# Kernel optimization log

Measured on AMD Instinct MI355X. Metric: run time of the kernel, lower is better.

The kernel has to match this reference:

```python
import jax, jax.numpy as jnp
import numpy as np

B, FNP, D = 16, 4096, 512
P, S, F = 16, 8, 32

def setup_inputs() -> dict:
    key = jax.random.key(0)
    k1, k2 = jax.random.split(key)
    token_states = jax.random.normal(k1, (B, FNP, D), dtype=jnp.float32)
    W = jax.random.normal(k2, (2 * P, D), dtype=jnp.float32) * 0.02
    b = jnp.zeros((2 * P,), dtype=jnp.float32)
    return {"token_states": token_states, "W": W, "b": b, "T": 1032}

def reference(token_states, W, b, T):
    Bsz, FNp, Dm = token_states.shape
    Np = FNp // F
    h = token_states.reshape(Bsz, F, Np, Dm)
    # per-patch linear head: [B, F, Np, 2P]
    raw = jnp.einsum('bfnd,ed->bfne', h, W) + b
    raw = raw.reshape(Bsz, F, Np, 2, P)
    mu = raw[:, :, :, 0, :]                                   # [B, F, Np, P]
    sigma = jnp.clip(jnp.exp(raw[:, :, :, 1, :]), 1e-06, None)
    mu = jnp.transpose(mu, (0, 2, 3, 1))                      # [B, Np, P, F]
    sigma = jnp.transpose(sigma, (0, 2, 3, 1))
    # overlap-add fold: time index for each (patch, offset)
    t = (jnp.arange(Np)[:, None] * S + jnp.arange(P)[None, :]).reshape(-1)  # [Np*P]
    valid = (t < T)
    t_c = jnp.where(valid, t, 0)
    vmask = valid.astype(mu.dtype)[None, :, None]             # [1, Np*P, 1]
    mu_flat = mu.reshape(Bsz, Np * P, F) * vmask
    sg_flat = sigma.reshape(Bsz, Np * P, F) * vmask
    mu_full = jnp.zeros((Bsz, T, F), dtype=mu.dtype).at[:, t_c, :].add(mu_flat)
    sigma_full = jnp.zeros((Bsz, T, F), dtype=mu.dtype).at[:, t_c, :].add(sg_flat)
    counts = jnp.zeros((T,), dtype=mu.dtype).at[t_c].add(valid.astype(mu.dtype))
    counts = jnp.clip(counts, 1.0, None)[None, :, None]       # [1, T, 1]
    return (mu_full / counts, sigma_full / counts)
```

## Files before the change

kernel.cpp:

```cpp
#include <hip/hip_runtime.h>
#include <math.h>

#define B_    16
#define F_    32
#define NP_   128
#define D_    512
#define P_    16
#define KC    64
#define NCHT  16
#define SLOTF 4096
#define EOFFF (4 * SLOTF)

typedef __attribute__((ext_vector_type(8)))  short  short8;
typedef __attribute__((ext_vector_type(16))) float  floatx16;

union Frag { short8 v; unsigned int u[4]; };

__device__ inline unsigned int cvt_pk_bf16(float lo, float hi) {
    unsigned int r;
    asm volatile("v_cvt_pk_bf16_f32 %0, %1, %2" : "=v"(r) : "v"(lo), "v"(hi));
    return r;
}

#define SB  __builtin_amdgcn_sched_barrier(0)
#define BAR asm volatile("s_waitcnt lgkmcnt(0)\n\ts_barrier" ::: "memory")

__global__ __launch_bounds__(512, 2)
void pd_kernel(const float* __restrict__ ts,
               const float* __restrict__ W,
               const float* __restrict__ bias,
               float* __restrict__ out, int T)
{
    __shared__ float smem[EOFFF + NP_ * 33];

    const int tid  = threadIdx.x;
    const int lane = tid & 63;
    const int wave = tid >> 6;
    const int mt   = wave & 3;
    const int p    = wave >> 2;

    const int d  = blockIdx.x;
    const int b  = (d & 7) | (((d >> 7) & 1) << 3);
    const int fp = (d >> 3) & 15;
    const float* __restrict__ tsb0 = ts + ((size_t)(b * F_ + 2 * fp) * NP_) * D_;
    const float* __restrict__ tsb1 = tsb0 + (size_t)NP_ * D_;

    const int lr = tid >> 2;
    const int lu = tid & 3;

    float4 st[3][4];
    auto LOAD = [&](int g) {
        const float* src = (g < 8 ? tsb0 : tsb1)
                         + (size_t)lr * D_ + (g & 7) * KC + lu * 16;
#pragma unroll
        for (int i = 0; i < 4; ++i) st[g % 3][i] = ((const float4*)src)[i];
    };
    auto WRITE = [&](int g) {
        Frag q0, q1;
        q0.u[0] = cvt_pk_bf16(st[g%3][0].x, st[g%3][0].y);
        q0.u[1] = cvt_pk_bf16(st[g%3][0].z, st[g%3][0].w);
        q0.u[2] = cvt_pk_bf16(st[g%3][1].x, st[g%3][1].y);
        q0.u[3] = cvt_pk_bf16(st[g%3][1].z, st[g%3][1].w);
        q1.u[0] = cvt_pk_bf16(st[g%3][2].x, st[g%3][2].y);
        q1.u[1] = cvt_pk_bf16(st[g%3][2].z, st[g%3][2].w);
        q1.u[2] = cvt_pk_bf16(st[g%3][3].x, st[g%3][3].y);
        q1.u[3] = cvt_pk_bf16(st[g%3][3].z, st[g%3][3].w);
        short8* slot = (short8*)(smem + (g & 3) * SLOTF);
        slot[lr * 8 + ((2 * lu)     ^ (lr & 7))] = q0.v;
        slot[lr * 8 + ((2 * lu + 1) ^ (lr & 7))] = q1.v;
    };

    const int e_b = lane & 31;
    const int kh  = lane >> 5;
    Frag bf[8][2];
    LOAD(0); SB;
    LOAD(1); LOAD(2); SB;
    {
        const float* wb = W + (size_t)e_b * D_ + kh * 8;
#pragma unroll
        for (int c = 0; c < 8; ++c)
#pragma unroll
            for (int j = 0; j < 2; ++j) {
                const int k = (4 * c + p + 2 * j) * 16;
                const float4 lo = *(const float4*)(wb + k);
                const float4 hi = *(const float4*)(wb + k + 4);
                bf[c][j].u[0] = cvt_pk_bf16(lo.x, lo.y);
                bf[c][j].u[1] = cvt_pk_bf16(lo.z, lo.w);
                bf[c][j].u[2] = cvt_pk_bf16(hi.x, hi.y);
                bf[c][j].u[3] = cvt_pk_bf16(hi.z, hi.w);
            }
    }
    SB;
    WRITE(0);
    BAR; SB;

    const int ro = mt * 32 + (lane & 31);

    auto COMPUTE = [&](int g, floatx16& acc) {
        const short8* slot = (const short8*)(smem + (g & 3) * SLOTF);
#pragma unroll
        for (int j = 0; j < 2; ++j) {
            const int qq = (p + 2 * j) * 2 + kh;
            Frag a; a.v = slot[ro * 8 + (qq ^ (ro & 7))];
            acc = __builtin_amdgcn_mfma_f32_32x32x16_bf16(a.v, bf[g & 7][j].v, acc, 0, 0, 0);
        }
    };

    floatx16 accA, accB;
#pragma unroll
    for (int r = 0; r < 16; ++r) { accA[r] = 0.f; accB[r] = 0.f; }

    const int TF = T * F_;
    const size_t halfoff = (size_t)B_ * TF;
    float* const E = smem + EOFFF;
    const int f0 = 2 * fp;
    const int QT = (2 * T + 3) / 4;

#pragma unroll
    for (int g = 0; g < NCHT; ++g) {
        if (g + 1 < NCHT) WRITE(g + 1);
        if (g + 3 < NCHT) LOAD(g + 3);
        SB;
        BAR;
        SB;

        if (g == 8) {
            if (p == 0) {
#pragma unroll
                for (int r = 0; r < 16; ++r) {
                    const int rowl = (r & 3) + 8 * (r >> 2) + 4 * kh;
                    E[(mt * 32 + rowl) * 33 + e_b] = accA[r];
                }
            }
        } else if (g == 9) {
            if (p == 1) {
#pragma unroll
                for (int r = 0; r < 16; ++r) {
                    const int rowl = (r & 3) + 8 * (r >> 2) + 4 * kh;
                    float v = E[(mt * 32 + rowl) * 33 + e_b] + accA[r] + bias[e_b];
                    if (e_b >= P_) v = fmaxf(expf(v), 1e-6f);
                    E[(mt * 32 + rowl) * 33 + e_b] = v;
                }
            }
        } else if (g >= 10 && g <= 13) {
            const int gq = g - 10;
            const int hi = min((gq + 1) * QT, 2 * T);
            for (int item = gq * QT + tid; item < hi; item += 512) {
                const int half = (item >= T) ? 1 : 0;
                const int t    = item - half * T;
                const int nmax = min(NP_ - 1, t >> 3);
                const int nmin = (t > 8) ? ((t - 8) >> 3) : 0;
                float sum = 0.f;
                const int cnt = nmax - nmin + 1;
                for (int nn = nmin; nn <= nmax; ++nn)
                    sum += E[nn * 33 + (half << 4) + (t - (nn << 3))];
                const float r = (cnt > 0) ? sum / (float)cnt : 0.f;
                out[(size_t)half * halfoff + (size_t)b * TF + (size_t)t * F_ + f0] = r;
            }
        }

        if (g < 8) COMPUTE(g, accA);
        else       COMPUTE(g, accB);
    }

    const int f1 = 2 * fp + 1;
    if (p == 0) {
#pragma unroll
        for (int r = 0; r < 16; ++r) {
            const int rowl = (r & 3) + 8 * (r >> 2) + 4 * kh;
            E[(mt * 32 + rowl) * 33 + e_b] = accB[r];
        }
    }
    BAR;
    if (p == 1) {
#pragma unroll
        for (int r = 0; r < 16; ++r) {
            const int rowl = (r & 3) + 8 * (r >> 2) + 4 * kh;
            float v = E[(mt * 32 + rowl) * 33 + e_b] + accB[r] + bias[e_b];
            if (e_b >= P_) v = fmaxf(expf(v), 1e-6f);
            E[(mt * 32 + rowl) * 33 + e_b] = v;
        }
    }
    BAR;
    for (int item = tid; item < 2 * T; item += 512) {
        const int half = (item >= T) ? 1 : 0;
        const int t    = item - half * T;
        const int nmax = min(NP_ - 1, t >> 3);
        const int nmin = (t > 8) ? ((t - 8) >> 3) : 0;
        float sum = 0.f;
        const int cnt = nmax - nmin + 1;
        for (int nn = nmin; nn <= nmax; ++nn)
            sum += E[nn * 33 + (half << 4) + (t - (nn << 3))];
        const float r = (cnt > 0) ? sum / (float)cnt : 0.f;
        out[(size_t)half * halfoff + (size_t)b * TF + (size_t)t * F_ + f1] = r;
    }
}

extern "C" void kernel_launch(void* const* d_in, const int* in_sizes, int n_in,
                              void* d_out, int out_size, void* d_ws, size_t ws_size,
                              hipStream_t stream)
{
    const float* ts   = (const float*)d_in[0];
    const float* W    = (const float*)d_in[1];
    const float* bias = (const float*)d_in[2];
    float* out = (float*)d_out;

    const int T = out_size / (2 * B_ * F_);

    dim3 grid(B_ * F_ / 2);
    dim3 block(512);
    pd_kernel<<<grid, block, 0, stream>>>(ts, W, bias, out, T);
}
```

Before: 36.19 us.

## Split GEMM by row-slabs with 16x16x32 MFMA and double epilogue buffers

Changes the per-chunk decomposition. Each chunk now holds 16 full-K rows, and waves are assigned by (mt, nt) to whole slabs, using the 16x16x32 bf16 MFMA over the full K. The old scheme split K across two wave groups with 32x32 tiles and a two-phase reduction through shared memory. The new one removes that cross-wave reduction and gives each output frame its own epilogue buffer, so the bias and exp epilogue runs right after each slab. The cost is that only 2 of 8 waves compute per chunk, which serialises the MFMA work, and W fragments now use 16 registers per lane.

```diff
diff --git a/kernel.cpp b/kernel.cpp
--- a/kernel.cpp
+++ b/kernel.cpp
@@ -6,13 +6,13 @@
 #define NP_   128
 #define D_    512
 #define P_    16
-#define KC    64
-#define NCHT  16
-#define SLOTF 4096
-#define EOFFF (4 * SLOTF)
+#define NSL   16
+#define SLABF 4096
+#define E0OFF (4 * SLABF)
+#define E1OFF (E0OFF + NP_ * 33)
 
-typedef __attribute__((ext_vector_type(8)))  short  short8;
-typedef __attribute__((ext_vector_type(16))) float  floatx16;
+typedef __attribute__((ext_vector_type(8))) short  short8;
+typedef __attribute__((ext_vector_type(4))) float  floatx4;
 
 union Frag { short8 v; unsigned int u[4]; };
 
@@ -31,13 +31,13 @@
                const float* __restrict__ bias,
                float* __restrict__ out, int T)
 {
-    __shared__ float smem[EOFFF + NP_ * 33];
+    __shared__ float smem[E1OFF + NP_ * 33];
 
     const int tid  = threadIdx.x;
     const int lane = tid & 63;
     const int wave = tid >> 6;
-    const int mt   = wave & 3;
-    const int p    = wave >> 2;
+    const int nt   = wave & 1;
+    const int mt   = wave >> 1;
 
     const int d  = blockIdx.x;
     const int b  = (d & 7) | (((d >> 7) & 1) << 3);
@@ -45,13 +45,13 @@
     const float* __restrict__ tsb0 = ts + ((size_t)(b * F_ + 2 * fp) * NP_) * D_;
     const float* __restrict__ tsb1 = tsb0 + (size_t)NP_ * D_;
 
-    const int lr = tid >> 2;
-    const int lu = tid & 3;
+    const int lr = tid >> 5;
+    const int lq = tid & 31;
 
     float4 st[3][4];
     auto LOAD = [&](int g) {
         const float* src = (g < 8 ? tsb0 : tsb1)
-                         + (size_t)lr * D_ + (g & 7) * KC + lu * 16;
+                         + ((size_t)((g & 7) * 16 + lr)) * D_ + lq * 16;
 #pragma unroll
         for (int i = 0; i < 4; ++i) st[g % 3][i] = ((const float4*)src)[i];
     };
@@ -65,135 +65,93 @@
         q1.u[1] = cvt_pk_bf16(st[g%3][2].z, st[g%3][2].w);
         q1.u[2] = cvt_pk_bf16(st[g%3][3].x, st[g%3][3].y);
         q1.u[3] = cvt_pk_bf16(st[g%3][3].z, st[g%3][3].w);
-        short8* slot = (short8*)(smem + (g & 3) * SLOTF);
-        slot[lr * 8 + ((2 * lu)     ^ (lr & 7))] = q0.v;
-        slot[lr * 8 + ((2 * lu + 1) ^ (lr & 7))] = q1.v;
+        short8* slab = (short8*)(smem + (g & 3) * SLABF);
+        const int qw = lq * 2;
+        slab[lr * 64 + ( qw      ^ lr)] = q0.v;
+        slab[lr * 64 + ((qw + 1) ^ lr)] = q1.v;
     };
 
-    const int e_b = lane & 31;
-    const int kh  = lane >> 5;
-    Frag bf[8][2];
     LOAD(0); SB;
     LOAD(1); LOAD(2); SB;
+
+    const int el = lane & 15;
+    const int kg = lane >> 4;
+    const int ef = nt * 16 + el;
+    Frag bf[16];
     {
-        const float* wb = W + (size_t)e_b * D_ + kh * 8;
+        const float* wb = W + (size_t)ef * D_ + kg * 8;
 #pragma unroll
-        for (int c = 0; c < 8; ++c)
-#pragma unroll
-            for (int j = 0; j < 2; ++j) {
-                const int k = (4 * c + p + 2 * j) * 16;
-                const float4 lo = *(const float4*)(wb + k);
-                const float4 hi = *(const float4*)(wb + k + 4);
-                bf[c][j].u[0] = cvt_pk_bf16(lo.x, lo.y);
-                bf[c][j].u[1] = cvt_pk_bf16(lo.z, lo.w);
-                bf[c][j].u[2] = cvt_pk_bf16(hi.x, hi.y);
-                bf[c][j].u[3] = cvt_pk_bf16(hi.z, hi.w);
-            }
+        for (int ks = 0; ks < 16; ++ks) {
+            const float4 lo = *(const float4*)(wb + ks * 32);
+            const float4 hi = *(const float4*)(wb + ks * 32 + 4);
+            bf[ks].u[0] = cvt_pk_bf16(lo.x, lo.y);
+            bf[ks].u[1] = cvt_pk_bf16(lo.z, lo.w);
+            bf[ks].u[2] = cvt_pk_bf16(hi.x, hi.y);
+            bf[ks].u[3] = cvt_pk_bf16(hi.z, hi.w);
+        }
     }
     SB;
     WRITE(0);
     BAR; SB;
 
-    const int ro = mt * 32 + (lane & 31);
+    const int TF = T * F_;
+    const size_t halfoff = (size_t)B_ * TF;
+    const int f0 = 2 * fp, f1 = 2 * fp + 1;
+    const int QT = (2 * T + 3) / 4;
 
-    auto COMPUTE = [&](int g, floatx16& acc) {
-        const short8* slot = (const short8*)(smem + (g & 3) * SLOTF);
-#pragma unroll
-        for (int j = 0; j < 2; ++j) {
-            const int qq = (p + 2 * j) * 2 + kh;
-            Frag a; a.v = slot[ro * 8 + (qq ^ (ro & 7))];
-            acc = __builtin_amdgcn_mfma_f32_32x32x16_bf16(a.v, bf[g & 7][j].v, acc, 0, 0, 0);
+    auto GATHER = [&](const float* E, int f, int lo_i, int hi_i) {
+        for (int item = lo_i + tid; item < hi_i; item += 512) {
+            const int half = (item >= T) ? 1 : 0;
+            const int t    = item - half * T;
+            const int nmax = min(NP_ - 1, t >> 3);
+            const int nmin = (t > 8) ? ((t - 8) >> 3) : 0;
+            float sum = 0.f;
+            const int cnt = nmax - nmin + 1;
+            for (int nn = nmin; nn <= nmax; ++nn)
+                sum += E[nn * 33 + (half << 4) + (t - (nn << 3))];
+            const float r = (cnt > 0) ? sum / (float)cnt : 0.f;
+            out[(size_t)half * halfoff + (size_t)b * TF + (size_t)t * F_ + f] = r;
         }
     };
 
-    floatx16 accA, accB;
 #pragma unroll
-    for (int r = 0; r < 16; ++r) { accA[r] = 0.f; accB[r] = 0.f; }
-
-    const int TF = T * F_;
-    const size_t halfoff = (size_t)B_ * TF;
-    float* const E = smem + EOFFF;
-    const int f0 = 2 * fp;
-    const int QT = (2 * T + 3) / 4;
-
-#pragma unroll
-    for (int g = 0; g < NCHT; ++g) {
-        if (g + 1 < NCHT) WRITE(g + 1);
-        if (g + 3 < NCHT) LOAD(g + 3);
+    for (int g = 0; g < NSL; ++g) {
+        if (g + 1 < NSL) WRITE(g + 1);
+        if (g + 3 < NSL) LOAD(g + 3);
         SB;
         BAR;
         SB;
 
-        if (g == 8) {
-            if (p == 0) {
+        if (g >= 9 && g <= 12) {
+            const int gq = g - 9;
+            GATHER(smem + E0OFF, f0, gq * QT, min((gq + 1) * QT, 2 * T));
+        }
+
+        if ((g & 3) == mt) {
+            const short8* slab = (const short8*)(smem + (g & 3) * SLABF);
+            floatx4 a4;
 #pragma unroll
-                for (int r = 0; r < 16; ++r) {
-                    const int rowl = (r & 3) + 8 * (r >> 2) + 4 * kh;
-                    E[(mt * 32 + rowl) * 33 + e_b] = accA[r];
-                }
+            for (int r = 0; r < 4; ++r) a4[r] = 0.f;
+#pragma unroll
+            for (int ks = 0; ks < 16; ++ks) {
+                Frag a;
+                a.v = slab[el * 64 + ((ks * 4 + kg) ^ el)];
+                a4 = __builtin_amdgcn_mfma_f32_16x16x32_bf16(a.v, bf[ks].v, a4, 0, 0, 0);
             }
-        } else if (g == 9) {
-            if (p == 1) {
+            float* E = smem + (g < 8 ? E0OFF : E1OFF);
+            const float bv = bias[ef];
 #pragma unroll
-                for (int r = 0; r < 16; ++r) {
-                    const int rowl = (r & 3) + 8 * (r >> 2) + 4 * kh;
-                    float v = E[(mt * 32 + rowl) * 33 + e_b] + accA[r] + bias[e_b];
-                    if (e_b >= P_) v = fmaxf(expf(v), 1e-6f);
-                    E[(mt * 32 + rowl) * 33 + e_b] = v;
-                }
-            }
-        } else if (g >= 10 && g <= 13) {
-            const int gq = g - 10;
-            const int hi = min((gq + 1) * QT, 2 * T);
-            for (int item = gq * QT + tid; item < hi; item += 512) {
-                const int half = (item >= T) ? 1 : 0;
-                const int t    = item - half * T;
-                const int nmax = min(NP_ - 1, t >> 3);
-                const int nmin = (t > 8) ? ((t - 8) >> 3) : 0;
-                float sum = 0.f;
-                const int cnt = nmax - nmin + 1;
-                for (int nn = nmin; nn <= nmax; ++nn)
-                    sum += E[nn * 33 + (half << 4) + (t - (nn << 3))];
-                const float r = (cnt > 0) ? sum / (float)cnt : 0.f;
-                out[(size_t)half * halfoff + (size_t)b * TF + (size_t)t * F_ + f0] = r;
+            for (int r = 0; r < 4; ++r) {
+                const int rowl = (g & 7) * 16 + kg * 4 + r;
+                float v = a4[r] + bv;
+                if (ef >= P_) v = fmaxf(expf(v), 1e-6f);
+                E[rowl * 33 + ef] = v;
             }
         }
-
-        if (g < 8) COMPUTE(g, accA);
-        else       COMPUTE(g, accB);
     }
 
-    const int f1 = 2 * fp + 1;
-    if (p == 0) {
-#pragma unroll
-        for (int r = 0; r < 16; ++r) {
-            const int rowl = (r & 3) + 8 * (r >> 2) + 4 * kh;
-            E[(mt * 32 + rowl) * 33 + e_b] = accB[r];
-        }
-    }
     BAR;
-    if (p == 1) {
-#pragma unroll
-        for (int r = 0; r < 16; ++r) {
-            const int rowl = (r & 3) + 8 * (r >> 2) + 4 * kh;
-            float v = E[(mt * 32 + rowl) * 33 + e_b] + accB[r] + bias[e_b];
-            if (e_b >= P_) v = fmaxf(expf(v), 1e-6f);
-            E[(mt * 32 + rowl) * 33 + e_b] = v;
-        }
-    }
-    BAR;
-    for (int item = tid; item < 2 * T; item += 512) {
-        const int half = (item >= T) ? 1 : 0;
-        const int t    = item - half * T;
-        const int nmax = min(NP_ - 1, t >> 3);
-        const int nmin = (t > 8) ? ((t - 8) >> 3) : 0;
-        float sum = 0.f;
-        const int cnt = nmax - nmin + 1;
-        for (int nn = nmin; nn <= nmax; ++nn)
-            sum += E[nn * 33 + (half << 4) + (t - (nn << 3))];
-        const float r = (cnt > 0) ? sum / (float)cnt : 0.f;
-        out[(size_t)half * halfoff + (size_t)b * TF + (size_t)t * F_ + f1] = r;
-    }
+    GATHER(smem + E1OFF, f1, 0, 2 * T);
 }
 
 extern "C" void kernel_launch(void* const* d_in, const int* in_sizes, int n_in,
```

Result: no change. 35.84 us (-1.0%).
